# Kernel optimization log

Measured on AMD Instinct MI355X. Metric: run time of the kernel, lower is better.

Reference implementation:

```python
import jax, jax.numpy as jnp
import numpy as np

R, C, B, E, H = 128, 256, 1, 768, 12
DK = E // H

def setup_inputs() -> dict:
    key = jax.random.key(0)
    ks = jax.random.split(key, 5)
    s = 1.0 / np.sqrt(E)
    return {
        "x": jax.random.normal(ks[0], (R, C, B, E), jnp.float32),
        "Wq": jax.random.normal(ks[1], (E, E), jnp.float32) * s,
        "bq": jnp.zeros((E,), jnp.float32),
        "Wk": jax.random.normal(ks[2], (E, E), jnp.float32) * s,
        "bk": jnp.zeros((E,), jnp.float32),
        "Wv": jax.random.normal(ks[3], (E, E), jnp.float32) * s,
        "bv": jnp.zeros((E,), jnp.float32),
        "Wo": jax.random.normal(ks[4], (E, E), jnp.float32) * s,
        "bo": jnp.zeros((E,), jnp.float32),
    }

def reference(x, Wq, bq, Wk, bk, Wv, bv, Wo, bo):
    n_rows, n_cols, batch, emb = x.shape
    scaling = (DK ** -0.5) / jnp.sqrt(jnp.float32(n_rows))
    # projections (torch Linear: x @ W.T + b)
    q = (x @ Wq.T + bq).reshape(n_rows, n_cols, batch, H, DK) * scaling
    k = (x @ Wk.T + bk).reshape(n_rows, n_cols, batch, H, DK)
    v = (x @ Wv.T + bv).reshape(n_rows, n_cols, batch, H, DK)
    # pooled attention logits: sum over rows r -> [H, B, C, C]
    attn = jnp.einsum('rinhd,rjnhd->hnij', q, k)
    probs = jax.nn.softmax(attn, axis=-1)  # single softmax shared across rows
    # context: [R, C, B, H, DK]
    c = jnp.einsum('hnij,rjnhd->rinhd', probs, v).reshape(n_rows, n_cols, batch, emb)
    out = c @ Wo.T + bo
    return out, probs
```

## Files before the change

### kernel.cpp

```cpp
#include <hip/hip_runtime.h>
#include <math.h>

#define R_  128
#define C_  256
#define E_  768
#define H_  12
#define DK_ 64
#define T_  (R_*C_)
#define RS_ 8
#define LP  40

typedef __attribute__((ext_vector_type(8))) short          bf16x8;
typedef __attribute__((ext_vector_type(4))) float          f32x4;
typedef __attribute__((ext_vector_type(4))) unsigned short u16x4;
typedef __attribute__((ext_vector_type(8))) unsigned short u16x8;

struct HL { unsigned short h, l; };

__device__ __forceinline__ HL split2(float f) {
    HL o;
    unsigned int u = __float_as_uint(f);
    o.h = (unsigned short)(u >> 16);
    float r = f - __uint_as_float(u & 0xFFFF0000u);
    o.l = (unsigned short)(__float_as_uint(r) >> 16);
    return o;
}

__device__ __forceinline__ void gload16(const void* g, void* l) {
    __builtin_amdgcn_global_load_lds(
        (const __attribute__((address_space(1))) unsigned int*)g,
        (__attribute__((address_space(3))) unsigned int*)l,
        16, 0, 0);
}

__global__ __launch_bounds__(256) void split_kernel(
    const float* __restrict__ src,
    unsigned short* __restrict__ h, unsigned short* __restrict__ l)
{
    const size_t i = ((size_t)blockIdx.x * 256 + threadIdx.x) * 8;
    float4 f0 = *(const float4*)(src + i);
    float4 f1 = *(const float4*)(src + i + 4);
    float v[8] = { f0.x, f0.y, f0.z, f0.w, f1.x, f1.y, f1.z, f1.w };
    u16x8 hh, ll;
    #pragma unroll
    for (int j = 0; j < 8; ++j) { HL e = split2(v[j]); hh[j] = e.h; ll[j] = e.l; }
    *(u16x8*)(h + i) = hh;
    *(u16x8*)(l + i) = ll;
}

template<int OMODE>
__global__ __launch_bounds__(256, 2) void gemm_kernel(
    const unsigned short* __restrict__ Ah, const unsigned short* __restrict__ Al,
    const unsigned short* __restrict__ Bh, const unsigned short* __restrict__ Bl,
    const float* __restrict__ bias, float scale,
    float* __restrict__ Y32, unsigned short* __restrict__ Yh, unsigned short* __restrict__ Yl)
{
    __shared__ __align__(16) unsigned short smem[2][16384];

    const int bid = blockIdx.x;
    const int swz = (bid & 7) * 192 + (bid >> 3);
    const int m0  = (swz / 6) * 128;
    const int n0  = (swz % 6) * 128;

    const int tid  = threadIdx.x;
    const int wave = tid >> 6, lane = tid & 63;
    const int wm   = (wave & 1) * 64, wn = (wave >> 1) * 64;
    const int fr   = lane & 15;
    const int kqs  = (((lane >> 4) ^ ((fr >> 1) & 3)) * 8);

    const int lrow = lane >> 2;
    const int gd   = (lane & 3) ^ ((lane >> 3) & 3);
    const unsigned short* gsrc = (wave == 0) ? Ah : (wave == 1) ? Al
                               : (wave == 2) ? Bh : Bl;
    const int rbase = (wave < 2) ? m0 : n0;
    const unsigned short* sp = gsrc + (size_t)(rbase + lrow) * E_ + 8 * gd;
    const int ltoff = wave * 4096;

    f32x4 acc[4][4] = {};

    {
        unsigned short* lt = &smem[0][ltoff];
        #pragma unroll
        for (int i = 0; i < 8; ++i)
            gload16(sp + (size_t)i * 16 * E_, lt + i * 512);
    }

    int cur = 0;
    for (int k0 = 0; k0 < E_; k0 += 32) {
        __syncthreads();
        if (k0 + 32 < E_) {
            unsigned short* lt = &smem[cur ^ 1][ltoff];
            #pragma unroll
            for (int i = 0; i < 8; ++i)
                gload16(sp + k0 + 32 + (size_t)i * 16 * E_, lt + i * 512);
        }
        const unsigned short* AsH = smem[cur];
        const unsigned short* AsL = smem[cur] + 4096;
        const unsigned short* BsH = smem[cur] + 8192;
        const unsigned short* BsL = smem[cur] + 12288;

        bf16x8 a_h[4], a_l[4], b_h[4], b_l[4];
        #pragma unroll
        for (int t = 0; t < 4; ++t) {
            a_h[t] = *(const bf16x8*)&AsH[(wm + t * 16 + fr) * 32 + kqs];
            a_l[t] = *(const bf16x8*)&AsL[(wm + t * 16 + fr) * 32 + kqs];
            b_h[t] = *(const bf16x8*)&BsH[(wn + t * 16 + fr) * 32 + kqs];
            b_l[t] = *(const bf16x8*)&BsL[(wn + t * 16 + fr) * 32 + kqs];
        }
        #pragma unroll
        for (int i = 0; i < 4; ++i)
            #pragma unroll
            for (int j = 0; j < 4; ++j) {
                acc[i][j] = __builtin_amdgcn_mfma_f32_16x16x32_bf16(a_h[i], b_h[j], acc[i][j], 0, 0, 0);
                acc[i][j] = __builtin_amdgcn_mfma_f32_16x16x32_bf16(a_h[i], b_l[j], acc[i][j], 0, 0, 0);
                acc[i][j] = __builtin_amdgcn_mfma_f32_16x16x32_bf16(a_l[i], b_h[j], acc[i][j], 0, 0, 0);
            }
        cur ^= 1;
    }

    float* rep = (float*)&smem[0][0] + wave * 1024;
    const int mr = lane >> 2;
    const int nc = (lane & 3) * 16;
    #pragma unroll
    for (int ti = 0; ti < 4; ++ti) {
        __syncthreads();
        #pragma unroll
        for (int tj = 0; tj < 4; ++tj)
            #pragma unroll
            for (int r = 0; r < 4; ++r)
                rep[((lane >> 4) * 4 + r) * 64 + tj * 16 + fr] = acc[ti][tj][r];
        __syncthreads();
        float v[16];
        #pragma unroll
        for (int c = 0; c < 4; ++c)
            *(float4*)&v[4 * c] = *(const float4*)&rep[mr * 64 + nc + 4 * c];
        const int gm = m0 + wm + ti * 16 + mr;
        const int gn = n0 + wn + nc;
        if constexpr (OMODE == 1) {
            #pragma unroll
            for (int c = 0; c < 4; ++c) {
                float4 bv = *(const float4*)&bias[gn + 4 * c];
                float4 o;
                o.x = (v[4*c+0] + bv.x) * scale; o.y = (v[4*c+1] + bv.y) * scale;
                o.z = (v[4*c+2] + bv.z) * scale; o.w = (v[4*c+3] + bv.w) * scale;
                *(float4*)&Y32[(size_t)gm * E_ + gn + 4 * c] = o;
            }
        } else {
            unsigned short hh[16], ll[16];
            #pragma unroll
            for (int c = 0; c < 4; ++c) {
                float4 bv = *(const float4*)&bias[gn + 4 * c];
                HL e0 = split2((v[4*c+0] + bv.x) * scale);
                HL e1 = split2((v[4*c+1] + bv.y) * scale);
                HL e2 = split2((v[4*c+2] + bv.z) * scale);
                HL e3 = split2((v[4*c+3] + bv.w) * scale);
                hh[4*c+0] = e0.h; ll[4*c+0] = e0.l;
                hh[4*c+1] = e1.h; ll[4*c+1] = e1.l;
                hh[4*c+2] = e2.h; ll[4*c+2] = e2.l;
                hh[4*c+3] = e3.h; ll[4*c+3] = e3.l;
            }
            u16x8 H0, H1, L0, L1;
            #pragma unroll
            for (int j = 0; j < 8; ++j) { H0[j] = hh[j]; H1[j] = hh[8+j]; L0[j] = ll[j]; L1[j] = ll[8+j]; }
            *(u16x8*)&Yh[(size_t)gm * E_ + gn]     = H0;
            *(u16x8*)&Yh[(size_t)gm * E_ + gn + 8] = H1;
            *(u16x8*)&Yl[(size_t)gm * E_ + gn]     = L0;
            *(u16x8*)&Yl[(size_t)gm * E_ + gn + 8] = L1;
        }
    }
}

__global__ __launch_bounds__(256, 2) void attn_mfma(
    const unsigned short* __restrict__ Qh, const unsigned short* __restrict__ Ql,
    const unsigned short* __restrict__ Kh, const unsigned short* __restrict__ Kl,
    float* __restrict__ part)
{
    __shared__ __align__(16) unsigned short smem[2][16384];

    const int bid = blockIdx.x;
    const int swz = (bid & 7) * 48 + (bid >> 3);
    const int hz  = swz >> 2;
    const int ij  = swz & 3;
    const int i0  = (ij & 1) * 128;
    const int j0  = (ij >> 1) * 128;
    const int h   = hz >> 3;
    const int rc  = hz & 7;

    const int tid  = threadIdx.x;
    const int wave = tid >> 6, lane = tid & 63;
    const int wm   = (wave & 1) * 64, wn = (wave >> 1) * 64;
    const int fr   = lane & 15;
    const int kqs  = (((lane >> 4) ^ ((fr >> 1) & 3)) * 8);

    const int lrow = lane >> 2;
    const int gd   = (lane & 3) ^ ((lane >> 3) & 3);
    const unsigned short* gsrc = (wave == 0) ? Qh : (wave == 1) ? Ql
                               : (wave == 2) ? Kh : Kl;
    const int rbase = (wave < 2) ? i0 : j0;
    const int ltoff = wave * 4096;
    const unsigned short* sp0 =
        gsrc + ((size_t)(rc * 16 * C_) + rbase + lrow) * E_ + h * DK_ + 8 * gd;

    f32x4 acc[4][4] = {};

    {
        unsigned short* lt = &smem[0][ltoff];
        #pragma unroll
        for (int i = 0; i < 8; ++i)
            gload16(sp0 + (size_t)i * 16 * E_, lt + i * 512);
    }

    int cur = 0;
    for (int s = 0; s < 32; ++s) {
        __syncthreads();
        if (s + 1 < 32) {
            const int sn = s + 1;
            const unsigned short* sp =
                sp0 + (size_t)(sn >> 1) * C_ * E_ + (sn & 1) * 32;
            unsigned short* lt = &smem[cur ^ 1][ltoff];
            #pragma unroll
            for (int i = 0; i < 8; ++i)
                gload16(sp + (size_t)i * 16 * E_, lt + i * 512);
        }
        const unsigned short* AsH = smem[cur];
        const unsigned short* AsL = smem[cur] + 4096;
        const unsigned short* BsH = smem[cur] + 8192;
        const unsigned short* BsL = smem[cur] + 12288;

        bf16x8 a_h[4], a_l[4], b_h[4], b_l[4];
        #pragma unroll
        for (int t = 0; t < 4; ++t) {
            a_h[t] = *(const bf16x8*)&AsH[(wm + t * 16 + fr) * 32 + kqs];
            a_l[t] = *(const bf16x8*)&AsL[(wm + t * 16 + fr) * 32 + kqs];
            b_h[t] = *(const bf16x8*)&BsH[(wn + t * 16 + fr) * 32 + kqs];
            b_l[t] = *(const bf16x8*)&BsL[(wn + t * 16 + fr) * 32 + kqs];
        }
        #pragma unroll
        for (int i = 0; i < 4; ++i)
            #pragma unroll
            for (int j = 0; j < 4; ++j) {
                acc[i][j] = __builtin_amdgcn_mfma_f32_16x16x32_bf16(a_h[i], b_h[j], acc[i][j], 0, 0, 0);
                acc[i][j] = __builtin_amdgcn_mfma_f32_16x16x32_bf16(a_h[i], b_l[j], acc[i][j], 0, 0, 0);
                acc[i][j] = __builtin_amdgcn_mfma_f32_16x16x32_bf16(a_l[i], b_h[j], acc[i][j], 0, 0, 0);
            }
        cur ^= 1;
    }

    float* rep = (float*)&smem[0][0] + wave * 1024;
    const int mr = lane >> 2;
    const int nc = (lane & 3) * 16;
    #pragma unroll
    for (int ti = 0; ti < 4; ++ti) {
        __syncthreads();
        #pragma unroll
        for (int tj = 0; tj < 4; ++tj)
            #pragma unroll
            for (int r = 0; r < 4; ++r)
                rep[((lane >> 4) * 4 + r) * 64 + tj * 16 + fr] = acc[ti][tj][r];
        __syncthreads();
        const int gi = i0 + wm + ti * 16 + mr;
        const int gj = j0 + wn + nc;
        #pragma unroll
        for (int c = 0; c < 4; ++c) {
            float4 o = *(const float4*)&rep[mr * 64 + nc + 4 * c];
            *(float4*)&part[((size_t)(rc * H_ + h) * C_ + gi) * C_ + gj + 4 * c] = o;
        }
    }
}

__global__ __launch_bounds__(256) void softmax_split(
    const float* __restrict__ part, float* __restrict__ probs,
    unsigned short* __restrict__ ph, unsigned short* __restrict__ pl)
{
    const int row = blockIdx.x;
    const int j = threadIdx.x;
    const int wave = j >> 6, lane = j & 63;

    float s = 0.0f;
    #pragma unroll
    for (int rcn = 0; rcn < RS_; ++rcn)
        s += part[((size_t)rcn * H_ * C_ + row) * C_ + j];

    float m = s;
    #pragma unroll
    for (int off = 32; off > 0; off >>= 1)
        m = fmaxf(m, __shfl_down(m, off, 64));
    __shared__ float redm[4];
    if (lane == 0) redm[wave] = m;
    __syncthreads();
    m = fmaxf(fmaxf(redm[0], redm[1]), fmaxf(redm[2], redm[3]));

    float e = expf(s - m);
    float t = e;
    #pragma unroll
    for (int off = 32; off > 0; off >>= 1)
        t += __shfl_down(t, off, 64);
    __shared__ float reds[4];
    if (lane == 0) reds[wave] = t;
    __syncthreads();
    t = reds[0] + reds[1] + reds[2] + reds[3];

    float p = e / t;
    probs[(size_t)row * C_ + j] = p;
    HL sp = split2(p);
    ph[(size_t)row * C_ + j] = sp.h;
    pl[(size_t)row * C_ + j] = sp.l;
}

__global__ __launch_bounds__(256, 2) void ctx_mfma(
    const unsigned short* __restrict__ Ph, const unsigned short* __restrict__ Pl,
    const unsigned short* __restrict__ Vh, const unsigned short* __restrict__ Vl,
    unsigned short* __restrict__ Ch, unsigned short* __restrict__ Cl)
{
    __shared__ __align__(16) unsigned short smem[2][13312];

    const int bid = blockIdx.x;
    const int swz = (bid & 7) * 384 + (bid >> 3);
    const int h   = swz >> 8;
    const int rem = swz & 255;
    const int r   = rem >> 1;
    const int i0  = (rem & 1) * 128;

    const int tid  = threadIdx.x;
    const int wave = tid >> 6, lane = tid & 63;
    const int wm   = (wave & 1) * 64, wn = (wave >> 1) * 32;
    const int fr   = lane & 15;
    const int kq   = (lane >> 4) * 8;
    const int kqs  = (((lane >> 4) ^ ((fr >> 1) & 3)) * 8);

    const int lrow   = lane >> 2;
    const int gd     = (lane & 3) ^ ((lane >> 3) & 3);
    const int pplane = wave >> 1;
    const int prhalf = (wave & 1) * 64;
    const unsigned short* psrc = (pplane ? Pl : Ph)
        + ((size_t)(h * C_) + i0 + prhalf + lrow) * C_ + 8 * gd;
    const int ptoff = pplane * 4096 + prhalf * 32;

    const int vjj = tid & 31;
    const int vdg = tid >> 5;
    const unsigned short* vhsrc = Vh + ((size_t)(r * C_) + vjj) * E_ + h * DK_ + vdg * 8;
    const unsigned short* vlsrc = Vl + ((size_t)(r * C_) + vjj) * E_ + h * DK_ + vdg * 8;

    f32x4 acc[4][2] = {};

    {
        #pragma unroll
        for (int i = 0; i < 4; ++i)
            gload16(psrc + (size_t)i * 16 * C_, &smem[0][ptoff + i * 512]);
        u16x8 v_h = *(const u16x8*)vhsrc;
        u16x8 v_l = *(const u16x8*)vlsrc;
        #pragma unroll
        for (int u = 0; u < 8; ++u) {
            smem[0][8192  + (vdg * 8 + u) * LP + vjj] = v_h[u];
            smem[0][10752 + (vdg * 8 + u) * LP + vjj] = v_l[u];
        }
    }

    for (int s = 0; s < 8; ++s) {
        const int cur = s & 1;
        __syncthreads();

        u16x8 v_h, v_l;
        const bool pf = (s + 1 < 8);
        if (pf) {
            const int jb = (s + 1) * 32;
            v_h = *(const u16x8*)(vhsrc + (size_t)jb * E_);
            v_l = *(const u16x8*)(vlsrc + (size_t)jb * E_);
            #pragma unroll
            for (int i = 0; i < 4; ++i)
                gload16(psrc + jb + (size_t)i * 16 * C_,
                        &smem[cur ^ 1][ptoff + i * 512]);
        }

        const unsigned short* PsH = smem[cur];
        const unsigned short* PsL = smem[cur] + 4096;
        const unsigned short* VsH = smem[cur] + 8192;
        const unsigned short* VsL = smem[cur] + 10752;

        bf16x8 p_h[4], p_l[4], w_h[2], w_l[2];
        #pragma unroll
        for (int t = 0; t < 4; ++t) {
            p_h[t] = *(const bf16x8*)&PsH[(wm + t * 16 + fr) * 32 + kqs];
            p_l[t] = *(const bf16x8*)&PsL[(wm + t * 16 + fr) * 32 + kqs];
        }
        #pragma unroll
        for (int t = 0; t < 2; ++t) {
            w_h[t] = *(const bf16x8*)&VsH[(wn + t * 16 + fr) * LP + kq];
            w_l[t] = *(const bf16x8*)&VsL[(wn + t * 16 + fr) * LP + kq];
        }
        #pragma unroll
        for (int i = 0; i < 4; ++i)
            #pragma unroll
            for (int j = 0; j < 2; ++j) {
                acc[i][j] = __builtin_amdgcn_mfma_f32_16x16x32_bf16(p_h[i], w_h[j], acc[i][j], 0, 0, 0);
                acc[i][j] = __builtin_amdgcn_mfma_f32_16x16x32_bf16(p_h[i], w_l[j], acc[i][j], 0, 0, 0);
                acc[i][j] = __builtin_amdgcn_mfma_f32_16x16x32_bf16(p_l[i], w_h[j], acc[i][j], 0, 0, 0);
            }

        if (pf) {
            #pragma unroll
            for (int u = 0; u < 8; ++u) {
                smem[cur ^ 1][8192  + (vdg * 8 + u) * LP + vjj] = v_h[u];
                smem[cur ^ 1][10752 + (vdg * 8 + u) * LP + vjj] = v_l[u];
            }
        }
    }

    float* rep = (float*)&smem[0][0] + wave * 512;
    const int mr = lane >> 2;
    const int nc = (lane & 3) * 8;
    #pragma unroll
    for (int ti = 0; ti < 4; ++ti) {
        __syncthreads();
        #pragma unroll
        for (int tj = 0; tj < 2; ++tj)
            #pragma unroll
            for (int rr = 0; rr < 4; ++rr)
                rep[((lane >> 4) * 4 + rr) * 32 + tj * 16 + fr] = acc[ti][tj][rr];
        __syncthreads();
        float v[8];
        *(float4*)&v[0] = *(const float4*)&rep[mr * 32 + nc];
        *(float4*)&v[4] = *(const float4*)&rep[mr * 32 + nc + 4];
        const int gm = r * C_ + i0 + wm + ti * 16 + mr;
        const int gn = h * DK_ + wn + nc;
        u16x8 H8, L8;
        #pragma unroll
        for (int jj = 0; jj < 8; ++jj) { HL e = split2(v[jj]); H8[jj] = e.h; L8[jj] = e.l; }
        *(u16x8*)&Ch[(size_t)gm * E_ + gn] = H8;
        *(u16x8*)&Cl[(size_t)gm * E_ + gn] = L8;
    }
}

extern "C" void kernel_launch(void* const* d_in, const int* in_sizes, int n_in,
                              void* d_out, int out_size, void* d_ws, size_t ws_size,
                              hipStream_t stream)
{
    (void)in_sizes; (void)n_in; (void)out_size; (void)ws_size;

    const float* x  = (const float*)d_in[0];
    const float* Wq = (const float*)d_in[1];
    const float* bq = (const float*)d_in[2];
    const float* Wk = (const float*)d_in[3];
    const float* bk = (const float*)d_in[4];
    const float* Wv = (const float*)d_in[5];
    const float* bv = (const float*)d_in[6];
    const float* Wo = (const float*)d_in[7];
    const float* bo = (const float*)d_in[8];

    float* out   = (float*)d_out;
    float* probs = out + (size_t)T_ * E_;
    float* part  = out;

    const size_t QN = (size_t)T_ * E_;
    const size_t WN = (size_t)E_ * E_;
    unsigned short* qh = (unsigned short*)d_ws;
    unsigned short* ql = qh + QN;
    unsigned short* kh = ql + QN;
    unsigned short* kl = kh + QN;
    unsigned short* vh = kl + QN;
    unsigned short* vl = vh + QN;
    unsigned short* ph = kh;
    unsigned short* pl = kh + (size_t)H_ * C_ * C_;
    unsigned short* ch = qh;
    unsigned short* cl = ql;

    unsigned short* xh   = (unsigned short*)out;
    unsigned short* xl   = xh + QN;
    unsigned short* wsph = (unsigned short*)probs;
    unsigned short* wspl = wsph + WN;
    unsigned short* woh  = kl;
    unsigned short* wol  = kl + WN;

    const float scaling = 0.125f / sqrtf(128.0f);

    dim3 blk(256);
    const int xblocks = (int)(QN / 2048);
    const int wblocks = (int)(WN / 2048);

    split_kernel<<<dim3(xblocks), blk, 0, stream>>>(x, xh, xl);

    split_kernel<<<dim3(wblocks), blk, 0, stream>>>(Wq, wsph, wspl);
    gemm_kernel<0><<<dim3(1536), blk, 0, stream>>>(
        xh, xl, wsph, wspl, bq, scaling, nullptr, qh, ql);

    split_kernel<<<dim3(wblocks), blk, 0, stream>>>(Wk, wsph, wspl);
    gemm_kernel<0><<<dim3(1536), blk, 0, stream>>>(
        xh, xl, wsph, wspl, bk, 1.0f, nullptr, kh, kl);

    split_kernel<<<dim3(wblocks), blk, 0, stream>>>(Wv, wsph, wspl);
    gemm_kernel<0><<<dim3(1536), blk, 0, stream>>>(
        xh, xl, wsph, wspl, bv, 1.0f, nullptr, vh, vl);

    attn_mfma<<<dim3(384), blk, 0, stream>>>(qh, ql, kh, kl, part);

    split_kernel<<<dim3(wblocks), blk, 0, stream>>>(Wo, woh, wol);

    softmax_split<<<dim3(H_ * C_), blk, 0, stream>>>(part, probs, ph, pl);
    ctx_mfma<<<dim3(3072), blk, 0, stream>>>(ph, pl, vh, vl, ch, cl);

    gemm_kernel<1><<<dim3(1536), blk, 0, stream>>>(
        ch, cl, woh, wol, bo, 1.0f, out, nullptr, nullptr);
}
```

Before: 851.0 us.

## Load GEMM B fragments directly from global into registers, halve LDS

The projection GEMM no longer stages the B operand (weights hi/lo) through shared memory. Each wave loads its B fragments straight from global memory into double-buffered registers, one k-step ahead, while only A is staged through LDS. LDS use per block is halved and launch bounds are raised to allow three blocks per CU, aiming for more occupancy and fewer LDS reads. The cost is uncoalesced, redundant global loads of B across waves and higher register pressure, which could cause spills under the tighter register budget.

```diff
diff --git a/kernel.cpp b/kernel.cpp
--- a/kernel.cpp
+++ b/kernel.cpp
@@ -49,13 +49,13 @@
 }
 
 template<int OMODE>
-__global__ __launch_bounds__(256, 2) void gemm_kernel(
+__global__ __launch_bounds__(256, 3) void gemm_kernel(
     const unsigned short* __restrict__ Ah, const unsigned short* __restrict__ Al,
     const unsigned short* __restrict__ Bh, const unsigned short* __restrict__ Bl,
     const float* __restrict__ bias, float scale,
     float* __restrict__ Y32, unsigned short* __restrict__ Yh, unsigned short* __restrict__ Yl)
 {
-    __shared__ __align__(16) unsigned short smem[2][16384];
+    __shared__ __align__(16) unsigned short smem[2][8192];
 
     const int bid = blockIdx.x;
     const int swz = (bid & 7) * 192 + (bid >> 3);
@@ -66,56 +66,70 @@
     const int wave = tid >> 6, lane = tid & 63;
     const int wm   = (wave & 1) * 64, wn = (wave >> 1) * 64;
     const int fr   = lane & 15;
+    const int kq   = (lane >> 4) * 8;
     const int kqs  = (((lane >> 4) ^ ((fr >> 1) & 3)) * 8);
 
-    const int lrow = lane >> 2;
-    const int gd   = (lane & 3) ^ ((lane >> 3) & 3);
-    const unsigned short* gsrc = (wave == 0) ? Ah : (wave == 1) ? Al
-                               : (wave == 2) ? Bh : Bl;
-    const int rbase = (wave < 2) ? m0 : n0;
-    const unsigned short* sp = gsrc + (size_t)(rbase + lrow) * E_ + 8 * gd;
-    const int ltoff = wave * 4096;
+    const int lrow  = lane >> 2;
+    const int gd    = (lane & 3) ^ ((lane >> 3) & 3);
+    const int rhalf = (wave & 1) * 64;
+    const unsigned short* asrc = ((wave >> 1) ? Al : Ah)
+                                 + (size_t)(m0 + rhalf + lrow) * E_ + 8 * gd;
+    const int ltoff = (wave >> 1) * 4096 + rhalf * 32;
+
+    const unsigned short* bhp = Bh + (size_t)(n0 + wn + fr) * E_ + kq;
+    const unsigned short* blp = Bl + (size_t)(n0 + wn + fr) * E_ + kq;
 
     f32x4 acc[4][4] = {};
-
-    {
-        unsigned short* lt = &smem[0][ltoff];
-        #pragma unroll
-        for (int i = 0; i < 8; ++i)
-            gload16(sp + (size_t)i * 16 * E_, lt + i * 512);
-    }
-
-    int cur = 0;
-    for (int k0 = 0; k0 < E_; k0 += 32) {
-        __syncthreads();
-        if (k0 + 32 < E_) {
-            unsigned short* lt = &smem[cur ^ 1][ltoff];
-            #pragma unroll
-            for (int i = 0; i < 8; ++i)
-                gload16(sp + k0 + 32 + (size_t)i * 16 * E_, lt + i * 512);
+    bf16x8 bA_h[4], bA_l[4], bB_h[4], bB_l[4];
+
+    #pragma unroll
+    for (int u = 0; u < 4; ++u) {
+        bA_h[u] = *(const bf16x8*)(bhp + (size_t)u * 16 * E_);
+        bA_l[u] = *(const bf16x8*)(blp + (size_t)u * 16 * E_);
+    }
+    #pragma unroll
+    for (int i = 0; i < 4; ++i)
+        gload16(asrc + (size_t)i * 16 * E_, &smem[0][ltoff + i * 512]);
+
+    const int NT = E_ / 32;
+
+    auto step = [&](int t, bf16x8 (&bu_h)[4], bf16x8 (&bu_l)[4],
+                           bf16x8 (&bp_h)[4], bf16x8 (&bp_l)[4]) {
+        const int cur = t & 1;
+        __syncthreads();
+        if (t + 1 < NT) {
+            const int k1 = (t + 1) * 32;
+            #pragma unroll
+            for (int u = 0; u < 4; ++u) {
+                bp_h[u] = *(const bf16x8*)(bhp + k1 + (size_t)u * 16 * E_);
+                bp_l[u] = *(const bf16x8*)(blp + k1 + (size_t)u * 16 * E_);
+            }
+            #pragma unroll
+            for (int i = 0; i < 4; ++i)
+                gload16(asrc + k1 + (size_t)i * 16 * E_,
+                        &smem[cur ^ 1][ltoff + i * 512]);
         }
         const unsigned short* AsH = smem[cur];
         const unsigned short* AsL = smem[cur] + 4096;
-        const unsigned short* BsH = smem[cur] + 8192;
-        const unsigned short* BsL = smem[cur] + 12288;
-
-        bf16x8 a_h[4], a_l[4], b_h[4], b_l[4];
-        #pragma unroll
-        for (int t = 0; t < 4; ++t) {
-            a_h[t] = *(const bf16x8*)&AsH[(wm + t * 16 + fr) * 32 + kqs];
-            a_l[t] = *(const bf16x8*)&AsL[(wm + t * 16 + fr) * 32 + kqs];
-            b_h[t] = *(const bf16x8*)&BsH[(wn + t * 16 + fr) * 32 + kqs];
-            b_l[t] = *(const bf16x8*)&BsL[(wn + t * 16 + fr) * 32 + kqs];
+        bf16x8 a_h[4], a_l[4];
+        #pragma unroll
+        for (int u = 0; u < 4; ++u) {
+            a_h[u] = *(const bf16x8*)&AsH[(wm + u * 16 + fr) * 32 + kqs];
+            a_l[u] = *(const bf16x8*)&AsL[(wm + u * 16 + fr) * 32 + kqs];
         }
         #pragma unroll
         for (int i = 0; i < 4; ++i)
             #pragma unroll
             for (int j = 0; j < 4; ++j) {
-                acc[i][j] = __builtin_amdgcn_mfma_f32_16x16x32_bf16(a_h[i], b_h[j], acc[i][j], 0, 0, 0);
-                acc[i][j] = __builtin_amdgcn_mfma_f32_16x16x32_bf16(a_h[i], b_l[j], acc[i][j], 0, 0, 0);
-                acc[i][j] = __builtin_amdgcn_mfma_f32_16x16x32_bf16(a_l[i], b_h[j], acc[i][j], 0, 0, 0);
-            }
-        cur ^= 1;
+                acc[i][j] = __builtin_amdgcn_mfma_f32_16x16x32_bf16(a_h[i], bu_h[j], acc[i][j], 0, 0, 0);
+                acc[i][j] = __builtin_amdgcn_mfma_f32_16x16x32_bf16(a_h[i], bu_l[j], acc[i][j], 0, 0, 0);
+                acc[i][j] = __builtin_amdgcn_mfma_f32_16x16x32_bf16(a_l[i], bu_h[j], acc[i][j], 0, 0, 0);
+            }
+    };
+
+    for (int t = 0; t < NT; t += 2) {
+        step(t,     bA_h, bA_l, bB_h, bB_l);
+        step(t + 1, bB_h, bB_l, bA_h, bA_l);
     }
 
     float* rep = (float*)&smem[0][0] + wave * 1024;
```

Measured after the change: 1.066 ms. 25.3% more time.
